# Optimization experiments

Hardware: AMD Instinct MI355X
Metric: run time of the kernel (lower is better)

## Reference

```python
import jax, jax.numpy as jnp
import numpy as np

FEAT = 256
HEADS = 8
HD = FEAT // HEADS
POS = 128
NEG = 128
H = 128
W = 128
B = 8
NSLOT = 512
LN_EPS = 1e-5


def setup_inputs() -> dict:
    key = jax.random.key(0)
    ks = jax.random.split(key, 8)
    HW = H * W
    features = jax.random.normal(ks[0], (HW, B, FEAT), dtype=jnp.float32)
    pos_encodings = jax.random.normal(ks[1], (HW, B, FEAT), dtype=jnp.float32)
    slots = jax.random.normal(ks[2], (1, NSLOT, FEAT), dtype=jnp.float32)
    curio_maps = jax.random.uniform(ks[3], (NSLOT, H, W), dtype=jnp.float32)
    batch_idx = jax.random.randint(ks[4], (NSLOT,), 0, B, dtype=jnp.int32)
    # parameters (xavier-ish scale)
    in_proj_weight = jax.random.normal(ks[5], (3 * FEAT, FEAT), dtype=jnp.float32) * 0.05
    in_proj_bias = jnp.zeros((3 * FEAT,), dtype=jnp.float32)
    out_w = jax.random.normal(ks[6], (FEAT, FEAT), dtype=jnp.float32) * 0.05
    out_b = jnp.zeros((FEAT,), dtype=jnp.float32)
    ln_g = jnp.ones((FEAT,), dtype=jnp.float32)
    ln_b = jnp.zeros((FEAT,), dtype=jnp.float32)
    return {
        'slots': slots, 'features': features, 'pos_encodings': pos_encodings,
        'curio_maps': curio_maps, 'batch_idx': batch_idx,
        'in_proj_weight': in_proj_weight, 'in_proj_bias': in_proj_bias,
        'out_w': out_w, 'out_b': out_b, 'ln_g': ln_g, 'ln_b': ln_b,
        'max_mask_entries': 0,
    }


def _sample_feat_idx(curio_maps, max_mask_entries):
    # curio_maps: [NSLOT, H, W] -> feat_idx: [POS+NEG, NSLOT]
    HW = curio_maps.shape[1] * curio_maps.shape[2]
    flat = curio_maps.reshape(NSLOT, HW)
    sorted_idx = jnp.argsort(-flat, axis=1)  # descending
    pos_idx = sorted_idx[:, :POS]
    pool = sorted_idx[:, POS:HW - max_mask_entries] if max_mask_entries > 0 else sorted_idx[:, POS:]
    # deterministic stand-in for random.sample: evenly-strided negatives
    stride = pool.shape[1] // NEG
    neg_idx = pool[:, ::stride][:, :NEG]
    return jnp.concatenate([pos_idx, neg_idx], axis=1).T  # [S, NSLOT]


def _forward(slots, features, pos_encodings, curio_maps, batch_idx,
             in_proj_weight, in_proj_bias, out_w, out_b, ln_g, ln_b,
             max_mask_entries):
    feat_idx = _sample_feat_idx(curio_maps, max_mask_entries)  # [S, NSLOT]
    S = feat_idx.shape[0]
    qw, kw, vw = in_proj_weight[:FEAT], in_proj_weight[FEAT:2 * FEAT], in_proj_weight[2 * FEAT:]
    qb, kb, vb = in_proj_bias[:FEAT], in_proj_bias[FEAT:2 * FEAT], in_proj_bias[2 * FEAT:]
    scaling = float(HD) ** -0.5
    # sample_type == 'after': project full maps, then gather
    q = (jnp.einsum('bnf,gf->bng', slots, qw) + qb) * scaling       # [1, NSLOT, FEAT]
    k = jnp.einsum('pbf,gf->pbg', features + pos_encodings, kw) + kb  # [HW, B, FEAT]
    v = jnp.einsum('pbf,gf->pbg', features, vw) + vb                  # [HW, B, FEAT]
    kg = k[feat_idx, batch_idx[None, :], :]            # [S, NSLOT, FEAT]
    vg = v[feat_idx[:POS], batch_idx[None, :], :]      # [POS, NSLOT, FEAT]
    qh = q.reshape(NSLOT, HEADS, HD)
    kh = kg.reshape(S, NSLOT, HEADS, HD)
    vh = vg.reshape(POS, NSLOT, HEADS, HD)
    affinities = jnp.einsum('nhd,snhd->snh', qh, kh)   # [S, NSLOT, HEADS]
    attn = jax.nn.softmax(affinities[:POS], axis=0)    # softmax over positive samples
    attn_out = jnp.einsum('pnh,pnhd->nhd', attn, vh).reshape(1, NSLOT, FEAT)
    attn_out = jnp.einsum('bnf,gf->bng', attn_out, out_w) + out_b
    x = slots + attn_out  # dropout is identity in eval
    mu = jnp.mean(x, axis=-1, keepdims=True)
    var = jnp.var(x, axis=-1, keepdims=True)
    new_slots = (x - mu) / jnp.sqrt(var + LN_EPS) * ln_g + ln_b
    return new_slots, affinities


def reference(slots, features, pos_encodings, curio_maps, batch_idx,
              in_proj_weight, in_proj_bias, out_w, out_b, ln_g, ln_b,
              max_mask_entries):
    return _forward(slots, features, pos_encodings, curio_maps, batch_idx,
                    in_proj_weight, in_proj_bias, out_w, out_b, ln_g, ln_b,
                    max_mask_entries)
```

## Files before the change

kernel.cpp:

```cpp
#include <hip/hip_runtime.h>
#include <hip/hip_bf16.h>

#define FEAT 256
#define HEADS 8
#define HD 32
#define POSN 128
#define NEGN 128
#define HWN 16384
#define BN 8
#define NSLOT 512
#define S_TOT 256
#define LN_EPS 1e-5f
#define NBKT 4096
#define AFF_OFF (NSLOT*FEAT)

typedef float f32x4 __attribute__((ext_vector_type(4)));

__global__ __launch_bounds__(256) void k_sample_qkw(const float* __restrict__ curio,
                                                    const int* __restrict__ mme_p,
                                                    const float* __restrict__ slots,
                                                    const float* __restrict__ ipw,
                                                    const float* __restrict__ ipb,
                                                    int* __restrict__ fi_t,
                                                    float* __restrict__ qkw,
                                                    float* __restrict__ qkb)
{
    __shared__ uint32_t hist[NBKT];
    __shared__ uint16_t offs[NBKT];
    __shared__ uint16_t sidx[HWN];
    __shared__ uint32_t ssum[256];
    __shared__ float srow[FEAT];
    __shared__ float qrow[FEAT];
    int slot = blockIdx.x, t = threadIdx.x;
    const float* cm = curio + (size_t)slot * HWN;
    const f32x4* cm4 = (const f32x4*)cm;

    for (int i = t; i < NBKT; i += 256) hist[i] = 0;
    __syncthreads();

    uint32_t bkA[16], bkB[16];
#pragma unroll
    for (int j = 0; j < 16; j++) {
        f32x4 v = cm4[j * 256 + t];
        int b0 = (int)(v[0] * 4096.0f); b0 = b0 < 0 ? 0 : (b0 > NBKT-1 ? NBKT-1 : b0);
        int b1 = (int)(v[1] * 4096.0f); b1 = b1 < 0 ? 0 : (b1 > NBKT-1 ? NBKT-1 : b1);
        int b2 = (int)(v[2] * 4096.0f); b2 = b2 < 0 ? 0 : (b2 > NBKT-1 ? NBKT-1 : b2);
        int b3 = (int)(v[3] * 4096.0f); b3 = b3 < 0 ? 0 : (b3 > NBKT-1 ? NBKT-1 : b3);
        bkA[j] = (uint32_t)b0 | ((uint32_t)b1 << 16);
        bkB[j] = (uint32_t)b2 | ((uint32_t)b3 << 16);
        atomicAdd(&hist[b0], 1u); atomicAdd(&hist[b1], 1u);
        atomicAdd(&hist[b2], 1u); atomicAdd(&hist[b3], 1u);
    }
    __syncthreads();

    uint32_t lsum = 0;
    int base = t * 16;
    for (int j = 0; j < 16; j++) lsum += hist[NBKT-1 - (base + j)];
    ssum[t] = lsum; __syncthreads();
    for (int off = 1; off < 256; off <<= 1) {
        uint32_t v = (t >= off) ? ssum[t - off] : 0u;
        __syncthreads();
        ssum[t] += v;
        __syncthreads();
    }
    uint32_t run = ssum[t] - lsum;
    for (int j = 0; j < 16; j++) {
        int b = NBKT-1 - (base + j);
        offs[b] = (uint16_t)run;
        run += hist[b];
    }
    __syncthreads();
    for (int i = t; i < NBKT; i += 256) hist[i] = 0;
    __syncthreads();

#pragma unroll
    for (int j = 0; j < 16; j++) {
        int idx0 = (j * 256 + t) * 4;
        int b0 = (int)(bkA[j] & 0xFFFFu), b1 = (int)(bkA[j] >> 16);
        int b2 = (int)(bkB[j] & 0xFFFFu), b3 = (int)(bkB[j] >> 16);
        uint32_t p0 = (uint32_t)offs[b0] + atomicAdd(&hist[b0], 1u);
        sidx[p0] = (uint16_t)(idx0 + 0);
        uint32_t p1 = (uint32_t)offs[b1] + atomicAdd(&hist[b1], 1u);
        sidx[p1] = (uint16_t)(idx0 + 1);
        uint32_t p2 = (uint32_t)offs[b2] + atomicAdd(&hist[b2], 1u);
        sidx[p2] = (uint16_t)(idx0 + 2);
        uint32_t p3 = (uint32_t)offs[b3] + atomicAdd(&hist[b3], 1u);
        sidx[p3] = (uint16_t)(idx0 + 3);
    }
    __syncthreads();

    int mme = mme_p[0];
    int stride = (HWN - POSN - mme) / NEGN;
    int r = (t < POSN) ? t : (POSN + stride * (t - POSN));
    int lo = 0, hi = NBKT - 1;
    while (lo < hi) { int mid = (lo + hi) >> 1; if ((int)offs[mid] <= r) hi = mid; else lo = mid + 1; }
    int bkt = lo;
    int start = (int)offs[bkt];
    int cnt   = (int)hist[bkt];
    int rr = r - start;
    int besti = sidx[start + (rr < cnt ? rr : 0)];
    for (int j = 0; j < cnt; j++) {
        int ij = sidx[start + j];
        float vj = cm[ij];
        int rank = 0;
        for (int j2 = 0; j2 < cnt; j2++) {
            int i2 = sidx[start + j2];
            float v2 = cm[i2];
            if (v2 > vj || (v2 == vj && i2 < ij)) rank++;
        }
        if (rank == rr) { besti = ij; break; }
    }
    fi_t[slot * S_TOT + t] = besti;

    __syncthreads();
    srow[t] = slots[slot * FEAT + t];
    __syncthreads();
    {
        const float* qwrow = ipw + (size_t)t * FEAT;
        float acc = 0.f;
#pragma unroll 8
        for (int f = 0; f < FEAT; f++) acc += srow[f] * qwrow[f];
        const float scaling = 0.17677669529663687f;
        qrow[t] = (acc + ipb[t]) * scaling;
    }
    __syncthreads();
    if (t < HEADS) {
        float s = 0.f;
        for (int d = 0; d < HD; d++) s += qrow[t*HD + d] * ipb[FEAT + t*HD + d];
        qkb[slot * HEADS + t] = s;
    }
    const float* kw = ipw + FEAT * FEAT;
    for (int e = t; e < HEADS * FEAT; e += 256) {
        int h = e >> 8, f = e & 255;
        float s = 0.f;
#pragma unroll
        for (int d = 0; d < HD; d++) s += qrow[h*HD + d] * kw[(h*HD + d) * FEAT + f];
        qkw[(size_t)slot * (HEADS*FEAT) + e] = s;
    }
}

__global__ __launch_bounds__(512, 2) void k_attn(const float* __restrict__ features,
                                                 const float* __restrict__ pos_enc,
                                                 const int* __restrict__ batch_idx,
                                                 const int* __restrict__ fi_t,
                                                 const float* __restrict__ qkw,
                                                 const float* __restrict__ qkb,
                                                 const float* __restrict__ slots,
                                                 const float* __restrict__ ipw,
                                                 const float* __restrict__ ipb,
                                                 const float* __restrict__ out_w,
                                                 const float* __restrict__ out_b,
                                                 const float* __restrict__ ln_g,
                                                 const float* __restrict__ ln_b,
                                                 float* __restrict__ aff_out,
                                                 float* __restrict__ out)
{
    __shared__ int   fi_l[S_TOT];
    __shared__ float qkb_l[HEADS];
    __shared__ __align__(16) float affP[POSN][8];
    __shared__ f32x4 wfp[4][HEADS][64];
    __shared__ f32x4 wf4[HEADS][64];
    __shared__ float aoh[512];
    __shared__ __align__(16) float ao_l[FEAT];
    __shared__ float xgh[512];
    __shared__ float r1[4], r2[4];

    int n = blockIdx.x, t = threadIdx.x, lane = t & 63, w = t >> 6;
    if (t < S_TOT) fi_l[t] = fi_t[n * S_TOT + t];
    if (t < HEADS) qkb_l[t] = qkb[n * HEADS + t];
    int b = batch_idx[n];

    const float* qk = qkw + (size_t)n * (HEADS*FEAT) + 4 * lane;
    f32x4 qw0 = *(const f32x4*)(qk + 0*FEAT);
    f32x4 qw1 = *(const f32x4*)(qk + 1*FEAT);
    f32x4 qw2 = *(const f32x4*)(qk + 2*FEAT);
    f32x4 qw3 = *(const f32x4*)(qk + 3*FEAT);
    f32x4 qw4 = *(const f32x4*)(qk + 4*FEAT);
    f32x4 qw5 = *(const f32x4*)(qk + 5*FEAT);
    f32x4 qw6 = *(const f32x4*)(qk + 6*FEAT);
    f32x4 qw7 = *(const f32x4*)(qk + 7*FEAT);
    __syncthreads();
    float qb = qkb_l[lane & 7];
    int b0 = lane & 1, b1 = (lane >> 1) & 1, b2 = (lane >> 2) & 1;

    auto dorow = [&](int p, f32x4 cf, f32x4 cg) {
        float x0 = cf[0]+cg[0], x1 = cf[1]+cg[1], x2 = cf[2]+cg[2], x3 = cf[3]+cg[3];
        float p0 = x0*qw0[0] + x1*qw0[1] + x2*qw0[2] + x3*qw0[3];
        float p1 = x0*qw1[0] + x1*qw1[1] + x2*qw1[2] + x3*qw1[3];
        float p2 = x0*qw2[0] + x1*qw2[1] + x2*qw2[2] + x3*qw2[3];
        float p3 = x0*qw3[0] + x1*qw3[1] + x2*qw3[2] + x3*qw3[3];
        float p4 = x0*qw4[0] + x1*qw4[1] + x2*qw4[2] + x3*qw4[3];
        float p5 = x0*qw5[0] + x1*qw5[1] + x2*qw5[2] + x3*qw5[3];
        float p6 = x0*qw6[0] + x1*qw6[1] + x2*qw6[2] + x3*qw6[3];
        float p7 = x0*qw7[0] + x1*qw7[1] + x2*qw7[2] + x3*qw7[3];
        float s0 = b0 ? p0 : p1, s1 = b0 ? p2 : p3, s2 = b0 ? p4 : p5, s3 = b0 ? p6 : p7;
        float a0 = (b0 ? p1 : p0) + __shfl_xor(s0, 1);
        float a1 = (b0 ? p3 : p2) + __shfl_xor(s1, 1);
        float a2 = (b0 ? p5 : p4) + __shfl_xor(s2, 1);
        float a3 = (b0 ? p7 : p6) + __shfl_xor(s3, 1);
        float u0 = b1 ? a0 : a1, u1 = b1 ? a2 : a3;
        float c0 = (b1 ? a1 : a0) + __shfl_xor(u0, 2);
        float c1 = (b1 ? a3 : a2) + __shfl_xor(u1, 2);
        float u2 = b2 ? c0 : c1;
        float d = (b2 ? c1 : c0) + __shfl_xor(u2, 4);
        d += __shfl_xor(d, 8);
        d += __shfl_xor(d, 16);
        d += __shfl_xor(d, 32);
        d += qb;
        if (lane < 8) {
            aff_out[(size_t)p * (NSLOT*HEADS) + n*HEADS + lane] = d;
            if (p < POSN) affP[p][lane] = d;
        }
    };

    f32x4 cache[16];
    size_t base0 = ((size_t)fi_l[w] * BN + b) * FEAT + 4 * lane;
    f32x4 f4 = *(const f32x4*)(features + base0);
    f32x4 g4 = *(const f32x4*)(pos_enc + base0);
#pragma unroll
    for (int i = 0; i < 16; i++) {
        f32x4 cf = f4, cg = g4;
        {
            size_t nb = ((size_t)fi_l[w + 8*(i+1)] * BN + b) * FEAT + 4 * lane;
            f4 = *(const f32x4*)(features + nb);
            g4 = *(const f32x4*)(pos_enc + nb);
        }
        cache[i] = cf;
        dorow(w + 8*i, cf, cg);
    }
#pragma unroll 4
    for (int i = 16; i < 32; i++) {
        f32x4 cf = f4, cg = g4;
        if (i < 31) {
            size_t nb = ((size_t)fi_l[w + 8*(i+1)] * BN + b) * FEAT + 4 * lane;
            f4 = *(const f32x4*)(features + nb);
            g4 = *(const f32x4*)(pos_enc + nb);
        }
        dorow(w + 8*i, cf, cg);
    }
    __syncthreads();

    if (t < 256) {
        int h = t >> 5, l = t & 31;
        float v0 = affP[l][h], v1 = affP[l+32][h], v2 = affP[l+64][h], v3 = affP[l+96][h];
        float m = fmaxf(fmaxf(v0, v1), fmaxf(v2, v3));
        for (int off = 16; off > 0; off >>= 1) m = fmaxf(m, __shfl_xor(m, off, 32));
        float e0 = expf(v0 - m), e1 = expf(v1 - m), e2 = expf(v2 - m), e3 = expf(v3 - m);
        float s = e0 + e1 + e2 + e3;
        for (int off = 16; off > 0; off >>= 1) s += __shfl_xor(s, off, 32);
        float inv = 1.0f / s;
        affP[l][h] = e0*inv; affP[l+32][h] = e1*inv; affP[l+64][h] = e2*inv; affP[l+96][h] = e3*inv;
    }
    __syncthreads();

    {
        f32x4 acc[8];
#pragma unroll
        for (int h = 0; h < 8; h++) acc[h] = (f32x4){0.f,0.f,0.f,0.f};
#pragma unroll
        for (int i = 0; i < 16; i++) {
            int p = w + 8*i;
            const f32x4* ap = (const f32x4*)&affP[p][0];
            f32x4 a03 = ap[0], a47 = ap[1];
            acc[0] += cache[i] * a03[0];
            acc[1] += cache[i] * a03[1];
            acc[2] += cache[i] * a03[2];
            acc[3] += cache[i] * a03[3];
            acc[4] += cache[i] * a47[0];
            acc[5] += cache[i] * a47[1];
            acc[6] += cache[i] * a47[2];
            acc[7] += cache[i] * a47[3];
        }
        if (w < 4) {
#pragma unroll
            for (int h = 0; h < 8; h++) wfp[w][h][lane] = acc[h];
        }
        __syncthreads();
        if (w >= 4) {
#pragma unroll
            for (int h = 0; h < 8; h++) wfp[w-4][h][lane] += acc[h];
        }
        __syncthreads();
    }
    {
        int h = t >> 6, q2 = t & 63;
        f32x4 s = wfp[0][h][q2] + wfp[1][h][q2] + wfp[2][h][q2] + wfp[3][h][q2];
        wf4[h][q2] = s;
    }
    __syncthreads();

    {
        int g = t & 255, half = t >> 8;
        const float* vwrow = ipw + (size_t)(2*FEAT + g) * FEAT + half*128;
        const f32x4* wfv = &wf4[g >> 5][half*32];
        float s = 0.f;
#pragma unroll 8
        for (int f4i = 0; f4i < 32; f4i++) {
            f32x4 wv = *(const f32x4*)(vwrow + 4*f4i);
            f32x4 y = wfv[f4i];
            s += wv[0]*y[0] + wv[1]*y[1] + wv[2]*y[2] + wv[3]*y[3];
        }
        aoh[t] = s;
    }
    __syncthreads();
    if (t < 256) ao_l[t] = aoh[t] + aoh[t + 256] + ipb[2*FEAT + t];
    __syncthreads();

    {
        int g = t & 255, half = t >> 8;
        const float* owrow = out_w + (size_t)g * FEAT + half*128;
        const f32x4* av = (const f32x4*)&ao_l[half*128];
        float s = 0.f;
#pragma unroll 8
        for (int f4i = 0; f4i < 32; f4i++) {
            f32x4 wv = *(const f32x4*)(owrow + 4*f4i);
            f32x4 y = av[f4i];
            s += wv[0]*y[0] + wv[1]*y[1] + wv[2]*y[2] + wv[3]*y[3];
        }
        xgh[t] = s;
    }
    __syncthreads();

    float xg = 0.f;
    if (t < 256) {
        xg = xgh[t] + xgh[t + 256] + out_b[t] + slots[n * FEAT + t];
        float s1 = xg, s2 = xg * xg;
        for (int off = 32; off > 0; off >>= 1) {
            s1 += __shfl_xor(s1, off);
            s2 += __shfl_xor(s2, off);
        }
        if ((t & 63) == 0) { r1[t >> 6] = s1; r2[t >> 6] = s2; }
    }
    __syncthreads();
    if (t < 256) {
        float sum1 = r1[0] + r1[1] + r1[2] + r1[3];
        float sum2 = r2[0] + r2[1] + r2[2] + r2[3];
        float mu  = sum1 * (1.0f / FEAT);
        float var = sum2 * (1.0f / FEAT) - mu * mu;
        float nrm = (xg - mu) * rsqrtf(var + LN_EPS);
        out[n * FEAT + t] = nrm * ln_g[t] + ln_b[t];
    }
}

extern "C" void kernel_launch(void* const* d_in, const int* in_sizes, int n_in,
                              void* d_out, int out_size, void* d_ws, size_t ws_size,
                              hipStream_t stream)
{
    (void)in_sizes; (void)n_in; (void)out_size; (void)ws_size;
    const float* slots    = (const float*)d_in[0];
    const float* features = (const float*)d_in[1];
    const float* pos_enc  = (const float*)d_in[2];
    const float* curio    = (const float*)d_in[3];
    const int*   batch_idx= (const int*)d_in[4];
    const float* ipw      = (const float*)d_in[5];
    const float* ipb      = (const float*)d_in[6];
    const float* out_w    = (const float*)d_in[7];
    const float* out_b    = (const float*)d_in[8];
    const float* ln_g     = (const float*)d_in[9];
    const float* ln_b     = (const float*)d_in[10];
    const int*   mme      = (const int*)d_in[11];
    float* out = (float*)d_out;

    char* ws = (char*)d_ws;
    int*   fi_t = (int*)ws;
    float* qkw  = (float*)(ws + (512 << 10));
    float* qkb  = (float*)(ws + (512 << 10) + (4 << 20));
    float* aff  = out + AFF_OFF;

    hipLaunchKernelGGL(k_sample_qkw, dim3(NSLOT), dim3(256), 0, stream,
                       curio, mme, slots, ipw, ipb, fi_t, qkw, qkb);
    hipLaunchKernelGGL(k_attn, dim3(NSLOT), dim3(512), 0, stream,
                       features, pos_enc, batch_idx, fi_t, qkw, qkb, slots, ipw, ipb,
                       out_w, out_b, ln_g, ln_b, aff, out);
}
```

Measured before the change: 132.6 us.

## Split attention kernel into positive and negative sample blocks per slot

The attention kernel now launches two blocks per slot. One block computes the affinities for the 128 negative samples and exits early, while the other handles the positive samples, softmax, value aggregation and layer norm. The gather loop is also restructured to keep two rows of loads in flight instead of one. This doubles parallelism and shortens the per-block critical path. The cost is redundant setup loads per block and extra pressure on registers and shared memory.

```diff
diff --git a/kernel.cpp b/kernel.cpp
--- a/kernel.cpp
+++ b/kernel.cpp
@@ -165,7 +165,9 @@
     __shared__ float xgh[512];
     __shared__ float r1[4], r2[4];
 
-    int n = blockIdx.x, t = threadIdx.x, lane = t & 63, w = t >> 6;
+    int bid = blockIdx.x;
+    int n = bid >> 1, kind = bid & 1;
+    int t = threadIdx.x, lane = t & 63, w = t >> 6;
     if (t < S_TOT) fi_l[t] = fi_t[n * S_TOT + t];
     if (t < HEADS) qkb_l[t] = qkb[n * HEADS + t];
     int b = batch_idx[n];
@@ -213,30 +215,57 @@
         }
     };
 
+    auto rowaddr = [&](int s) {
+        return ((size_t)fi_l[s] * BN + b) * FEAT + 4 * lane;
+    };
+
+    if (kind) {
+        int base_s = POSN + w;
+        size_t aA = rowaddr(base_s);
+        size_t aB = rowaddr(base_s + 8);
+        f32x4 fA = *(const f32x4*)(features + aA), gA = *(const f32x4*)(pos_enc + aA);
+        f32x4 fB = *(const f32x4*)(features + aB), gB = *(const f32x4*)(pos_enc + aB);
+#pragma unroll
+        for (int i = 0; i < 16; i += 2) {
+            f32x4 cf = fA, cg = gA;
+            if (i + 2 < 16) {
+                size_t nb = rowaddr(base_s + 8*(i+2));
+                fA = *(const f32x4*)(features + nb); gA = *(const f32x4*)(pos_enc + nb);
+            }
+            dorow(base_s + 8*i, cf, cg);
+            f32x4 cf2 = fB, cg2 = gB;
+            if (i + 3 < 16) {
+                size_t nb = rowaddr(base_s + 8*(i+3));
+                fB = *(const f32x4*)(features + nb); gB = *(const f32x4*)(pos_enc + nb);
+            }
+            dorow(base_s + 8*(i+1), cf2, cg2);
+        }
+        return;
+    }
+
     f32x4 cache[16];
-    size_t base0 = ((size_t)fi_l[w] * BN + b) * FEAT + 4 * lane;
-    f32x4 f4 = *(const f32x4*)(features + base0);
-    f32x4 g4 = *(const f32x4*)(pos_enc + base0);
-#pragma unroll
-    for (int i = 0; i < 16; i++) {
-        f32x4 cf = f4, cg = g4;
-        {
-            size_t nb = ((size_t)fi_l[w + 8*(i+1)] * BN + b) * FEAT + 4 * lane;
-            f4 = *(const f32x4*)(features + nb);
-            g4 = *(const f32x4*)(pos_enc + nb);
-        }
-        cache[i] = cf;
-        dorow(w + 8*i, cf, cg);
-    }
-#pragma unroll 4
-    for (int i = 16; i < 32; i++) {
-        f32x4 cf = f4, cg = g4;
-        if (i < 31) {
-            size_t nb = ((size_t)fi_l[w + 8*(i+1)] * BN + b) * FEAT + 4 * lane;
-            f4 = *(const f32x4*)(features + nb);
-            g4 = *(const f32x4*)(pos_enc + nb);
-        }
-        dorow(w + 8*i, cf, cg);
+    {
+        size_t aA = rowaddr(w);
+        size_t aB = rowaddr(w + 8);
+        f32x4 fA = *(const f32x4*)(features + aA), gA = *(const f32x4*)(pos_enc + aA);
+        f32x4 fB = *(const f32x4*)(features + aB), gB = *(const f32x4*)(pos_enc + aB);
+#pragma unroll
+        for (int i = 0; i < 16; i += 2) {
+            f32x4 cf = fA, cg = gA;
+            if (i + 2 < 16) {
+                size_t nb = rowaddr(w + 8*(i+2));
+                fA = *(const f32x4*)(features + nb); gA = *(const f32x4*)(pos_enc + nb);
+            }
+            cache[i] = cf;
+            dorow(w + 8*i, cf, cg);
+            f32x4 cf2 = fB, cg2 = gB;
+            if (i + 3 < 16) {
+                size_t nb = rowaddr(w + 8*(i+3));
+                fB = *(const f32x4*)(features + nb); gB = *(const f32x4*)(pos_enc + nb);
+            }
+            cache[i+1] = cf2;
+            dorow(w + 8*(i+1), cf2, cg2);
+        }
     }
     __syncthreads();
 
@@ -369,7 +398,7 @@
 
     hipLaunchKernelGGL(k_sample_qkw, dim3(NSLOT), dim3(256), 0, stream,
                        curio, mme, slots, ipw, ipb, fi_t, qkw, qkb);
-    hipLaunchKernelGGL(k_attn, dim3(NSLOT), dim3(512), 0, stream,
+    hipLaunchKernelGGL(k_attn, dim3(2 * NSLOT), dim3(512), 0, stream,
                        features, pos_enc, batch_idx, fi_t, qkw, qkb, slots, ipw, ipb,
                        out_w, out_b, ln_g, ln_b, aff, out);
 }
```

New measurement: 166.1 us. 25.2% more time.

## Invert affinity gather into streaming pass over feature rows with bucketed requests

Applied to the files above, without the earlier changes.

Rather than each slot block gathering 256 random feature and pos_enc rows, the sampling kernel now records, for every (pixel, batch) key, the list of (slot, sample) requests. A new streaming kernel walks all feature rows in order, loads each requested row once and computes the affinity for every request attached to it. Requests beyond the per-key capacity go through a spill list. The output kernel then reloads the affinities and the positive feature rows. The aim is to turn scattered, duplicated gathers into coalesced sequential reads with reuse. The cost is global atomics, two memsets, an extra kernel launch and extra aff round-trips, and the stream pass scans all 131k keys even though many have no requests.

```diff
diff --git a/kernel.cpp b/kernel.cpp
--- a/kernel.cpp
+++ b/kernel.cpp
@@ -13,6 +13,12 @@
 #define LN_EPS 1e-5f
 #define NBKT 4096
 #define AFF_OFF (NSLOT*FEAT)
+#define NKEY (HWN*BN)
+#define CAP 16
+#define SPILL_MAX 4096
+#define ROWS_PER_WAVE 8
+#define STREAM_ROW_BLOCKS 4096
+#define SPILL_BLOCKS 8
 
 typedef float f32x4 __attribute__((ext_vector_type(4)));
 
@@ -21,14 +27,19 @@
                                                     const float* __restrict__ slots,
                                                     const float* __restrict__ ipw,
                                                     const float* __restrict__ ipb,
+                                                    const int* __restrict__ batch_idx,
                                                     int* __restrict__ fi_t,
                                                     float* __restrict__ qkw,
-                                                    float* __restrict__ qkb)
+                                                    float* __restrict__ qkb,
+                                                    unsigned int* __restrict__ counts,
+                                                    unsigned int* __restrict__ entries,
+                                                    unsigned int* __restrict__ spill_cnt,
+                                                    unsigned long long* __restrict__ spills)
 {
-    __shared__ uint32_t hist[NBKT];
+    __shared__ unsigned int hist[NBKT];
     __shared__ uint16_t offs[NBKT];
     __shared__ uint16_t sidx[HWN];
-    __shared__ uint32_t ssum[256];
+    __shared__ unsigned int ssum[256];
     __shared__ float srow[FEAT];
     __shared__ float qrow[FEAT];
     int slot = blockIdx.x, t = threadIdx.x;
@@ -38,7 +49,7 @@
     for (int i = t; i < NBKT; i += 256) hist[i] = 0;
     __syncthreads();
 
-    uint32_t bkA[16], bkB[16];
+    unsigned int bkA[16], bkB[16];
 #pragma unroll
     for (int j = 0; j < 16; j++) {
         f32x4 v = cm4[j * 256 + t];
@@ -46,24 +57,24 @@
         int b1 = (int)(v[1] * 4096.0f); b1 = b1 < 0 ? 0 : (b1 > NBKT-1 ? NBKT-1 : b1);
         int b2 = (int)(v[2] * 4096.0f); b2 = b2 < 0 ? 0 : (b2 > NBKT-1 ? NBKT-1 : b2);
         int b3 = (int)(v[3] * 4096.0f); b3 = b3 < 0 ? 0 : (b3 > NBKT-1 ? NBKT-1 : b3);
-        bkA[j] = (uint32_t)b0 | ((uint32_t)b1 << 16);
-        bkB[j] = (uint32_t)b2 | ((uint32_t)b3 << 16);
+        bkA[j] = (unsigned int)b0 | ((unsigned int)b1 << 16);
+        bkB[j] = (unsigned int)b2 | ((unsigned int)b3 << 16);
         atomicAdd(&hist[b0], 1u); atomicAdd(&hist[b1], 1u);
         atomicAdd(&hist[b2], 1u); atomicAdd(&hist[b3], 1u);
     }
     __syncthreads();
 
-    uint32_t lsum = 0;
+    unsigned int lsum = 0;
     int base = t * 16;
     for (int j = 0; j < 16; j++) lsum += hist[NBKT-1 - (base + j)];
     ssum[t] = lsum; __syncthreads();
     for (int off = 1; off < 256; off <<= 1) {
-        uint32_t v = (t >= off) ? ssum[t - off] : 0u;
+        unsigned int v = (t >= off) ? ssum[t - off] : 0u;
         __syncthreads();
         ssum[t] += v;
         __syncthreads();
     }
-    uint32_t run = ssum[t] - lsum;
+    unsigned int run = ssum[t] - lsum;
     for (int j = 0; j < 16; j++) {
         int b = NBKT-1 - (base + j);
         offs[b] = (uint16_t)run;
@@ -78,13 +89,13 @@
         int idx0 = (j * 256 + t) * 4;
         int b0 = (int)(bkA[j] & 0xFFFFu), b1 = (int)(bkA[j] >> 16);
         int b2 = (int)(bkB[j] & 0xFFFFu), b3 = (int)(bkB[j] >> 16);
-        uint32_t p0 = (uint32_t)offs[b0] + atomicAdd(&hist[b0], 1u);
+        unsigned int p0 = (unsigned int)offs[b0] + atomicAdd(&hist[b0], 1u);
         sidx[p0] = (uint16_t)(idx0 + 0);
-        uint32_t p1 = (uint32_t)offs[b1] + atomicAdd(&hist[b1], 1u);
+        unsigned int p1 = (unsigned int)offs[b1] + atomicAdd(&hist[b1], 1u);
         sidx[p1] = (uint16_t)(idx0 + 1);
-        uint32_t p2 = (uint32_t)offs[b2] + atomicAdd(&hist[b2], 1u);
+        unsigned int p2 = (unsigned int)offs[b2] + atomicAdd(&hist[b2], 1u);
         sidx[p2] = (uint16_t)(idx0 + 2);
-        uint32_t p3 = (uint32_t)offs[b3] + atomicAdd(&hist[b3], 1u);
+        unsigned int p3 = (unsigned int)offs[b3] + atomicAdd(&hist[b3], 1u);
         sidx[p3] = (uint16_t)(idx0 + 3);
     }
     __syncthreads();
@@ -112,6 +123,20 @@
     }
     fi_t[slot * S_TOT + t] = besti;
 
+    {
+        int b = batch_idx[slot];
+        int key = besti * BN + b;
+        unsigned int payload = ((unsigned int)slot << 8) | (unsigned int)t;
+        unsigned int c = atomicAdd(&counts[key], 1u);
+        if (c < CAP) {
+            entries[(size_t)key * CAP + c] = payload;
+        } else {
+            unsigned int sp = atomicAdd(spill_cnt, 1u);
+            if (sp < SPILL_MAX)
+                spills[sp] = ((unsigned long long)payload << 32) | (unsigned int)key;
+        }
+    }
+
     __syncthreads();
     srow[t] = slots[slot * FEAT + t];
     __syncthreads();
@@ -139,37 +164,13 @@
     }
 }
 
-__global__ __launch_bounds__(512, 2) void k_attn(const float* __restrict__ features,
-                                                 const float* __restrict__ pos_enc,
-                                                 const int* __restrict__ batch_idx,
-                                                 const int* __restrict__ fi_t,
-                                                 const float* __restrict__ qkw,
-                                                 const float* __restrict__ qkb,
-                                                 const float* __restrict__ slots,
-                                                 const float* __restrict__ ipw,
-                                                 const float* __restrict__ ipb,
-                                                 const float* __restrict__ out_w,
-                                                 const float* __restrict__ out_b,
-                                                 const float* __restrict__ ln_g,
-                                                 const float* __restrict__ ln_b,
-                                                 float* __restrict__ aff_out,
-                                                 float* __restrict__ out)
+__device__ __forceinline__ void ref_affinity(const float* __restrict__ qkw,
+                                             const float* __restrict__ qkb,
+                                             float* __restrict__ aff_out,
+                                             f32x4 xs, unsigned int payload,
+                                             int lane, int b0, int b1, int b2)
 {
-    __shared__ int   fi_l[S_TOT];
-    __shared__ float qkb_l[HEADS];
-    __shared__ __align__(16) float affP[POSN][8];
-    __shared__ f32x4 wfp[4][HEADS][64];
-    __shared__ f32x4 wf4[HEADS][64];
-    __shared__ float aoh[512];
-    __shared__ __align__(16) float ao_l[FEAT];
-    __shared__ float xgh[512];
-    __shared__ float r1[4], r2[4];
-
-    int n = blockIdx.x, t = threadIdx.x, lane = t & 63, w = t >> 6;
-    if (t < S_TOT) fi_l[t] = fi_t[n * S_TOT + t];
-    if (t < HEADS) qkb_l[t] = qkb[n * HEADS + t];
-    int b = batch_idx[n];
-
+    int n = (int)(payload >> 8), s = (int)(payload & 255u);
     const float* qk = qkw + (size_t)n * (HEADS*FEAT) + 4 * lane;
     f32x4 qw0 = *(const f32x4*)(qk + 0*FEAT);
     f32x4 qw1 = *(const f32x4*)(qk + 1*FEAT);
@@ -179,66 +180,152 @@
     f32x4 qw5 = *(const f32x4*)(qk + 5*FEAT);
     f32x4 qw6 = *(const f32x4*)(qk + 6*FEAT);
     f32x4 qw7 = *(const f32x4*)(qk + 7*FEAT);
-    __syncthreads();
-    float qb = qkb_l[lane & 7];
+    float qb = qkb[n * HEADS + (lane & 7)];
+    float p0 = xs[0]*qw0[0] + xs[1]*qw0[1] + xs[2]*qw0[2] + xs[3]*qw0[3];
+    float p1 = xs[0]*qw1[0] + xs[1]*qw1[1] + xs[2]*qw1[2] + xs[3]*qw1[3];
+    float p2 = xs[0]*qw2[0] + xs[1]*qw2[1] + xs[2]*qw2[2] + xs[3]*qw2[3];
+    float p3 = xs[0]*qw3[0] + xs[1]*qw3[1] + xs[2]*qw3[2] + xs[3]*qw3[3];
+    float p4 = xs[0]*qw4[0] + xs[1]*qw4[1] + xs[2]*qw4[2] + xs[3]*qw4[3];
+    float p5 = xs[0]*qw5[0] + xs[1]*qw5[1] + xs[2]*qw5[2] + xs[3]*qw5[3];
+    float p6 = xs[0]*qw6[0] + xs[1]*qw6[1] + xs[2]*qw6[2] + xs[3]*qw6[3];
+    float p7 = xs[0]*qw7[0] + xs[1]*qw7[1] + xs[2]*qw7[2] + xs[3]*qw7[3];
+    float s0 = b0 ? p0 : p1, s1 = b0 ? p2 : p3, s2 = b0 ? p4 : p5, s3 = b0 ? p6 : p7;
+    float a0 = (b0 ? p1 : p0) + __shfl_xor(s0, 1);
+    float a1 = (b0 ? p3 : p2) + __shfl_xor(s1, 1);
+    float a2 = (b0 ? p5 : p4) + __shfl_xor(s2, 1);
+    float a3 = (b0 ? p7 : p6) + __shfl_xor(s3, 1);
+    float u0 = b1 ? a0 : a1, u1 = b1 ? a2 : a3;
+    float c0 = (b1 ? a1 : a0) + __shfl_xor(u0, 2);
+    float c1 = (b1 ? a3 : a2) + __shfl_xor(u1, 2);
+    float u2 = b2 ? c0 : c1;
+    float d = (b2 ? c1 : c0) + __shfl_xor(u2, 4);
+    d += __shfl_xor(d, 8);
+    d += __shfl_xor(d, 16);
+    d += __shfl_xor(d, 32);
+    d += qb;
+    if (lane < 8)
+        aff_out[(size_t)s * (NSLOT*HEADS) + n*HEADS + lane] = d;
+}
+
+__global__ __launch_bounds__(256) void k_stream_aff(const float* __restrict__ features,
+                                                    const float* __restrict__ pos_enc,
+                                                    const float* __restrict__ qkw,
+                                                    const float* __restrict__ qkb,
+                                                    const unsigned int* __restrict__ counts,
+                                                    const unsigned int* __restrict__ entries,
+                                                    const unsigned int* __restrict__ spill_cnt,
+                                                    const unsigned long long* __restrict__ spills,
+                                                    float* __restrict__ aff_out)
+{
+    int t = threadIdx.x, lane = t & 63, w = t >> 6;
     int b0 = lane & 1, b1 = (lane >> 1) & 1, b2 = (lane >> 2) & 1;
 
-    auto dorow = [&](int p, f32x4 cf, f32x4 cg) {
-        float x0 = cf[0]+cg[0], x1 = cf[1]+cg[1], x2 = cf[2]+cg[2], x3 = cf[3]+cg[3];
-        float p0 = x0*qw0[0] + x1*qw0[1] + x2*qw0[2] + x3*qw0[3];
-        float p1 = x0*qw1[0] + x1*qw1[1] + x2*qw1[2] + x3*qw1[3];
-        float p2 = x0*qw2[0] + x1*qw2[1] + x2*qw2[2] + x3*qw2[3];
-        float p3 = x0*qw3[0] + x1*qw3[1] + x2*qw3[2] + x3*qw3[3];
-        float p4 = x0*qw4[0] + x1*qw4[1] + x2*qw4[2] + x3*qw4[3];
-        float p5 = x0*qw5[0] + x1*qw5[1] + x2*qw5[2] + x3*qw5[3];
-        float p6 = x0*qw6[0] + x1*qw6[1] + x2*qw6[2] + x3*qw6[3];
-        float p7 = x0*qw7[0] + x1*qw7[1] + x2*qw7[2] + x3*qw7[3];
-        float s0 = b0 ? p0 : p1, s1 = b0 ? p2 : p3, s2 = b0 ? p4 : p5, s3 = b0 ? p6 : p7;
-        float a0 = (b0 ? p1 : p0) + __shfl_xor(s0, 1);
-        float a1 = (b0 ? p3 : p2) + __shfl_xor(s1, 1);
-        float a2 = (b0 ? p5 : p4) + __shfl_xor(s2, 1);
-        float a3 = (b0 ? p7 : p6) + __shfl_xor(s3, 1);
-        float u0 = b1 ? a0 : a1, u1 = b1 ? a2 : a3;
-        float c0 = (b1 ? a1 : a0) + __shfl_xor(u0, 2);
-        float c1 = (b1 ? a3 : a2) + __shfl_xor(u1, 2);
-        float u2 = b2 ? c0 : c1;
-        float d = (b2 ? c1 : c0) + __shfl_xor(u2, 4);
-        d += __shfl_xor(d, 8);
-        d += __shfl_xor(d, 16);
-        d += __shfl_xor(d, 32);
-        d += qb;
-        if (lane < 8) {
-            aff_out[(size_t)p * (NSLOT*HEADS) + n*HEADS + lane] = d;
-            if (p < POSN) affP[p][lane] = d;
-        }
-    };
+    if (blockIdx.x >= STREAM_ROW_BLOCKS) {
+        unsigned int nsp = *spill_cnt;
+        if (nsp > SPILL_MAX) nsp = SPILL_MAX;
+        unsigned int start = (blockIdx.x - STREAM_ROW_BLOCKS) * 4 + w;
+        for (unsigned int k = start; k < nsp; k += SPILL_BLOCKS * 4) {
+            unsigned long long e = spills[k];
+            unsigned int key = (unsigned int)e;
+            unsigned int payload = (unsigned int)(e >> 32);
+            const float* fp = features + (size_t)key * FEAT + 4 * lane;
+            const float* gp = pos_enc  + (size_t)key * FEAT + 4 * lane;
+            f32x4 cf = *(const f32x4*)fp;
+            f32x4 cg = *(const f32x4*)gp;
+            ref_affinity(qkw, qkb, aff_out, cf + cg, payload, lane, b0, b1, b2);
+        }
+        return;
+    }
+
+    int gw = blockIdx.x * 4 + w;
+    int r0 = gw * ROWS_PER_WAVE;
+
+    int takes[ROWS_PER_WAVE];
+#pragma unroll
+    for (int i = 0; i < ROWS_PER_WAVE; i++) {
+        unsigned int c = counts[r0 + i];
+        takes[i] = (int)(c < CAP ? c : CAP);
+    }
+
+    int cur = 0;
+    while (cur < ROWS_PER_WAVE && takes[cur] == 0) cur++;
+    f32x4 f4 = {0,0,0,0}, g4 = {0,0,0,0};
+    if (cur < ROWS_PER_WAVE) {
+        const float* fp = features + (size_t)(r0 + cur) * FEAT + 4 * lane;
+        const float* gp = pos_enc  + (size_t)(r0 + cur) * FEAT + 4 * lane;
+        f4 = *(const f32x4*)fp; g4 = *(const f32x4*)gp;
+    }
+    while (cur < ROWS_PER_WAVE) {
+        int nx = cur + 1;
+        while (nx < ROWS_PER_WAVE && takes[nx] == 0) nx++;
+        f32x4 cf = f4, cg = g4;
+        if (nx < ROWS_PER_WAVE) {
+            const float* fp = features + (size_t)(r0 + nx) * FEAT + 4 * lane;
+            const float* gp = pos_enc  + (size_t)(r0 + nx) * FEAT + 4 * lane;
+            f4 = *(const f32x4*)fp; g4 = *(const f32x4*)gp;
+        }
+        f32x4 xs = cf + cg;
+        const unsigned int* ebase = entries + (size_t)(r0 + cur) * CAP;
+        int tk = takes[cur];
+        for (int j = 0; j < tk; j++)
+            ref_affinity(qkw, qkb, aff_out, xs, ebase[j], lane, b0, b1, b2);
+        cur = nx;
+    }
+}
+
+__global__ __launch_bounds__(512, 2) void k_out(const float* __restrict__ features,
+                                                const int* __restrict__ batch_idx,
+                                                const int* __restrict__ fi_t,
+                                                const float* __restrict__ slots,
+                                                const float* __restrict__ ipw,
+                                                const float* __restrict__ ipb,
+                                                const float* __restrict__ out_w,
+                                                const float* __restrict__ out_b,
+                                                const float* __restrict__ ln_g,
+                                                const float* __restrict__ ln_b,
+                                                const float* __restrict__ aff,
+                                                float* __restrict__ out)
+{
+    __shared__ int   fiP[POSN];
+    __shared__ __align__(16) float affP[POSN][8];
+    __shared__ f32x4 wfp[4][HEADS][64];
+    __shared__ f32x4 wf4[HEADS][64];
+    __shared__ float aoh[512];
+    __shared__ __align__(16) float ao_l[FEAT];
+    __shared__ float xgh[512];
+    __shared__ float r1[4], r2[4];
+
+    int n = blockIdx.x, t = threadIdx.x, lane = t & 63, w = t >> 6;
+    if (t < POSN) fiP[t] = fi_t[n * S_TOT + t];
+    for (int e = t; e < POSN * HEADS; e += 512) {
+        int p = e >> 3, h = e & 7;
+        affP[p][h] = aff[(size_t)p * (NSLOT*HEADS) + n*HEADS + h];
+    }
+    int b = batch_idx[n];
+    __syncthreads();
 
     f32x4 cache[16];
-    size_t base0 = ((size_t)fi_l[w] * BN + b) * FEAT + 4 * lane;
-    f32x4 f4 = *(const f32x4*)(features + base0);
-    f32x4 g4 = *(const f32x4*)(pos_enc + base0);
-#pragma unroll
-    for (int i = 0; i < 16; i++) {
-        f32x4 cf = f4, cg = g4;
-        {
-            size_t nb = ((size_t)fi_l[w + 8*(i+1)] * BN + b) * FEAT + 4 * lane;
-            f4 = *(const f32x4*)(features + nb);
-            g4 = *(const f32x4*)(pos_enc + nb);
-        }
-        cache[i] = cf;
-        dorow(w + 8*i, cf, cg);
-    }
-#pragma unroll 4
-    for (int i = 16; i < 32; i++) {
-        f32x4 cf = f4, cg = g4;
-        if (i < 31) {
-            size_t nb = ((size_t)fi_l[w + 8*(i+1)] * BN + b) * FEAT + 4 * lane;
-            f4 = *(const f32x4*)(features + nb);
-            g4 = *(const f32x4*)(pos_enc + nb);
-        }
-        dorow(w + 8*i, cf, cg);
-    }
-    __syncthreads();
+    {
+        size_t aA = ((size_t)fiP[w] * BN + b) * FEAT + 4 * lane;
+        size_t aB = ((size_t)fiP[w + 8] * BN + b) * FEAT + 4 * lane;
+        f32x4 fA = *(const f32x4*)(features + aA);
+        f32x4 fB = *(const f32x4*)(features + aB);
+#pragma unroll
+        for (int i = 0; i < 16; i += 2) {
+            f32x4 c0 = fA;
+            if (i + 2 < 16) {
+                size_t nb = ((size_t)fiP[w + 8*(i+2)] * BN + b) * FEAT + 4 * lane;
+                fA = *(const f32x4*)(features + nb);
+            }
+            cache[i] = c0;
+            f32x4 c1 = fB;
+            if (i + 3 < 16) {
+                size_t nb = ((size_t)fiP[w + 8*(i+3)] * BN + b) * FEAT + 4 * lane;
+                fB = *(const f32x4*)(features + nb);
+            }
+            cache[i+1] = c1;
+        }
+    }
 
     if (t < 256) {
         int h = t >> 5, l = t & 31;
@@ -362,14 +449,31 @@
     float* out = (float*)d_out;
 
     char* ws = (char*)d_ws;
+    const size_t OFF_QKW = 512u << 10;
+    const size_t OFF_QKB = OFF_QKW + (4u << 20);
+    const size_t OFF_CNT = OFF_QKB + (64u << 10);
+    const size_t OFF_ENT = OFF_CNT + (512u << 10);
+    const size_t OFF_SPC = OFF_ENT + ((size_t)NKEY * CAP * 4);
+    const size_t OFF_SPL = OFF_SPC + 1024;
+
     int*   fi_t = (int*)ws;
-    float* qkw  = (float*)(ws + (512 << 10));
-    float* qkb  = (float*)(ws + (512 << 10) + (4 << 20));
+    float* qkw  = (float*)(ws + OFF_QKW);
+    float* qkb  = (float*)(ws + OFF_QKB);
+    unsigned int* counts = (unsigned int*)(ws + OFF_CNT);
+    unsigned int* entries = (unsigned int*)(ws + OFF_ENT);
+    unsigned int* spill_cnt = (unsigned int*)(ws + OFF_SPC);
+    unsigned long long* spills = (unsigned long long*)(ws + OFF_SPL);
     float* aff  = out + AFF_OFF;
 
+    hipMemsetAsync(counts, 0, (512u << 10) + 0, stream);
+    hipMemsetAsync(spill_cnt, 0, 1024, stream);
+
     hipLaunchKernelGGL(k_sample_qkw, dim3(NSLOT), dim3(256), 0, stream,
-                       curio, mme, slots, ipw, ipb, fi_t, qkw, qkb);
-    hipLaunchKernelGGL(k_attn, dim3(NSLOT), dim3(512), 0, stream,
-                       features, pos_enc, batch_idx, fi_t, qkw, qkb, slots, ipw, ipb,
+                       curio, mme, slots, ipw, ipb, batch_idx,
+                       fi_t, qkw, qkb, counts, entries, spill_cnt, spills);
+    hipLaunchKernelGGL(k_stream_aff, dim3(STREAM_ROW_BLOCKS + SPILL_BLOCKS), dim3(256), 0, stream,
+                       features, pos_enc, qkw, qkb, counts, entries, spill_cnt, spills, aff);
+    hipLaunchKernelGGL(k_out, dim3(NSLOT), dim3(512), 0, stream,
+                       features, batch_idx, fi_t, slots, ipw, ipb,
                        out_w, out_b, ln_g, ln_b, aff, out);
 }
```

After: 177.9 us. 34.2% more time.

## Split attention kernel into affinity and output kernels with deeper prefetch

Applied to the files above, without the earlier changes.

Splits the fused attention kernel into two. The first computes all 256 affinities per slot over a 2x512 grid of 256-thread blocks, using a double-buffered four-row prefetch. The second reads the positive affinities back from global memory, re-gathers the feature rows it needs for the value path, and then does softmax, output projection and layernorm. The aim is more parallelism and more memory-level parallelism in the gather-heavy affinity stage. In exchange it adds a kernel launch, a global round-trip of the affinities, and a second gather of the positive feature rows.

```diff
diff --git a/kernel.cpp b/kernel.cpp
--- a/kernel.cpp
+++ b/kernel.cpp
@@ -25,10 +25,10 @@
                                                     float* __restrict__ qkw,
                                                     float* __restrict__ qkb)
 {
-    __shared__ uint32_t hist[NBKT];
+    __shared__ unsigned int hist[NBKT];
     __shared__ uint16_t offs[NBKT];
     __shared__ uint16_t sidx[HWN];
-    __shared__ uint32_t ssum[256];
+    __shared__ unsigned int ssum[256];
     __shared__ float srow[FEAT];
     __shared__ float qrow[FEAT];
     int slot = blockIdx.x, t = threadIdx.x;
@@ -38,7 +38,7 @@
     for (int i = t; i < NBKT; i += 256) hist[i] = 0;
     __syncthreads();
 
-    uint32_t bkA[16], bkB[16];
+    unsigned int bkA[16], bkB[16];
 #pragma unroll
     for (int j = 0; j < 16; j++) {
         f32x4 v = cm4[j * 256 + t];
@@ -46,24 +46,24 @@
         int b1 = (int)(v[1] * 4096.0f); b1 = b1 < 0 ? 0 : (b1 > NBKT-1 ? NBKT-1 : b1);
         int b2 = (int)(v[2] * 4096.0f); b2 = b2 < 0 ? 0 : (b2 > NBKT-1 ? NBKT-1 : b2);
         int b3 = (int)(v[3] * 4096.0f); b3 = b3 < 0 ? 0 : (b3 > NBKT-1 ? NBKT-1 : b3);
-        bkA[j] = (uint32_t)b0 | ((uint32_t)b1 << 16);
-        bkB[j] = (uint32_t)b2 | ((uint32_t)b3 << 16);
+        bkA[j] = (unsigned int)b0 | ((unsigned int)b1 << 16);
+        bkB[j] = (unsigned int)b2 | ((unsigned int)b3 << 16);
         atomicAdd(&hist[b0], 1u); atomicAdd(&hist[b1], 1u);
         atomicAdd(&hist[b2], 1u); atomicAdd(&hist[b3], 1u);
     }
     __syncthreads();
 
-    uint32_t lsum = 0;
+    unsigned int lsum = 0;
     int base = t * 16;
     for (int j = 0; j < 16; j++) lsum += hist[NBKT-1 - (base + j)];
     ssum[t] = lsum; __syncthreads();
     for (int off = 1; off < 256; off <<= 1) {
-        uint32_t v = (t >= off) ? ssum[t - off] : 0u;
+        unsigned int v = (t >= off) ? ssum[t - off] : 0u;
         __syncthreads();
         ssum[t] += v;
         __syncthreads();
     }
-    uint32_t run = ssum[t] - lsum;
+    unsigned int run = ssum[t] - lsum;
     for (int j = 0; j < 16; j++) {
         int b = NBKT-1 - (base + j);
         offs[b] = (uint16_t)run;
@@ -78,13 +78,13 @@
         int idx0 = (j * 256 + t) * 4;
         int b0 = (int)(bkA[j] & 0xFFFFu), b1 = (int)(bkA[j] >> 16);
         int b2 = (int)(bkB[j] & 0xFFFFu), b3 = (int)(bkB[j] >> 16);
-        uint32_t p0 = (uint32_t)offs[b0] + atomicAdd(&hist[b0], 1u);
+        unsigned int p0 = (unsigned int)offs[b0] + atomicAdd(&hist[b0], 1u);
         sidx[p0] = (uint16_t)(idx0 + 0);
-        uint32_t p1 = (uint32_t)offs[b1] + atomicAdd(&hist[b1], 1u);
+        unsigned int p1 = (unsigned int)offs[b1] + atomicAdd(&hist[b1], 1u);
         sidx[p1] = (uint16_t)(idx0 + 1);
-        uint32_t p2 = (uint32_t)offs[b2] + atomicAdd(&hist[b2], 1u);
+        unsigned int p2 = (unsigned int)offs[b2] + atomicAdd(&hist[b2], 1u);
         sidx[p2] = (uint16_t)(idx0 + 2);
-        uint32_t p3 = (uint32_t)offs[b3] + atomicAdd(&hist[b3], 1u);
+        unsigned int p3 = (unsigned int)offs[b3] + atomicAdd(&hist[b3], 1u);
         sidx[p3] = (uint16_t)(idx0 + 3);
     }
     __syncthreads();
@@ -139,34 +139,20 @@
     }
 }
 
-__global__ __launch_bounds__(512, 2) void k_attn(const float* __restrict__ features,
-                                                 const float* __restrict__ pos_enc,
-                                                 const int* __restrict__ batch_idx,
-                                                 const int* __restrict__ fi_t,
-                                                 const float* __restrict__ qkw,
-                                                 const float* __restrict__ qkb,
-                                                 const float* __restrict__ slots,
-                                                 const float* __restrict__ ipw,
-                                                 const float* __restrict__ ipb,
-                                                 const float* __restrict__ out_w,
-                                                 const float* __restrict__ out_b,
-                                                 const float* __restrict__ ln_g,
-                                                 const float* __restrict__ ln_b,
-                                                 float* __restrict__ aff_out,
-                                                 float* __restrict__ out)
+__global__ __launch_bounds__(256) void k_aff(const float* __restrict__ features,
+                                             const float* __restrict__ pos_enc,
+                                             const int* __restrict__ batch_idx,
+                                             const int* __restrict__ fi_t,
+                                             const float* __restrict__ qkw,
+                                             const float* __restrict__ qkb,
+                                             float* __restrict__ aff_out)
 {
-    __shared__ int   fi_l[S_TOT];
+    __shared__ int   fi_l[128];
     __shared__ float qkb_l[HEADS];
-    __shared__ __align__(16) float affP[POSN][8];
-    __shared__ f32x4 wfp[4][HEADS][64];
-    __shared__ f32x4 wf4[HEADS][64];
-    __shared__ float aoh[512];
-    __shared__ __align__(16) float ao_l[FEAT];
-    __shared__ float xgh[512];
-    __shared__ float r1[4], r2[4];
-
-    int n = blockIdx.x, t = threadIdx.x, lane = t & 63, w = t >> 6;
-    if (t < S_TOT) fi_l[t] = fi_t[n * S_TOT + t];
+    int n = blockIdx.y, q = blockIdx.x;
+    int t = threadIdx.x, lane = t & 63, w = t >> 6;
+
+    if (t < 128) fi_l[t] = fi_t[n * S_TOT + q * 128 + t];
     if (t < HEADS) qkb_l[t] = qkb[n * HEADS + t];
     int b = batch_idx[n];
 
@@ -183,16 +169,15 @@
     float qb = qkb_l[lane & 7];
     int b0 = lane & 1, b1 = (lane >> 1) & 1, b2 = (lane >> 2) & 1;
 
-    auto dorow = [&](int p, f32x4 cf, f32x4 cg) {
-        float x0 = cf[0]+cg[0], x1 = cf[1]+cg[1], x2 = cf[2]+cg[2], x3 = cf[3]+cg[3];
-        float p0 = x0*qw0[0] + x1*qw0[1] + x2*qw0[2] + x3*qw0[3];
-        float p1 = x0*qw1[0] + x1*qw1[1] + x2*qw1[2] + x3*qw1[3];
-        float p2 = x0*qw2[0] + x1*qw2[1] + x2*qw2[2] + x3*qw2[3];
-        float p3 = x0*qw3[0] + x1*qw3[1] + x2*qw3[2] + x3*qw3[3];
-        float p4 = x0*qw4[0] + x1*qw4[1] + x2*qw4[2] + x3*qw4[3];
-        float p5 = x0*qw5[0] + x1*qw5[1] + x2*qw5[2] + x3*qw5[3];
-        float p6 = x0*qw6[0] + x1*qw6[1] + x2*qw6[2] + x3*qw6[3];
-        float p7 = x0*qw7[0] + x1*qw7[1] + x2*qw7[2] + x3*qw7[3];
+    auto dorow = [&](int s, f32x4 x) {
+        float p0 = x[0]*qw0[0] + x[1]*qw0[1] + x[2]*qw0[2] + x[3]*qw0[3];
+        float p1 = x[0]*qw1[0] + x[1]*qw1[1] + x[2]*qw1[2] + x[3]*qw1[3];
+        float p2 = x[0]*qw2[0] + x[1]*qw2[1] + x[2]*qw2[2] + x[3]*qw2[3];
+        float p3 = x[0]*qw3[0] + x[1]*qw3[1] + x[2]*qw3[2] + x[3]*qw3[3];
+        float p4 = x[0]*qw4[0] + x[1]*qw4[1] + x[2]*qw4[2] + x[3]*qw4[3];
+        float p5 = x[0]*qw5[0] + x[1]*qw5[1] + x[2]*qw5[2] + x[3]*qw5[3];
+        float p6 = x[0]*qw6[0] + x[1]*qw6[1] + x[2]*qw6[2] + x[3]*qw6[3];
+        float p7 = x[0]*qw7[0] + x[1]*qw7[1] + x[2]*qw7[2] + x[3]*qw7[3];
         float s0 = b0 ? p0 : p1, s1 = b0 ? p2 : p3, s2 = b0 ? p4 : p5, s3 = b0 ? p6 : p7;
         float a0 = (b0 ? p1 : p0) + __shfl_xor(s0, 1);
         float a1 = (b0 ? p3 : p2) + __shfl_xor(s1, 1);
@@ -207,38 +192,75 @@
         d += __shfl_xor(d, 16);
         d += __shfl_xor(d, 32);
         d += qb;
-        if (lane < 8) {
-            aff_out[(size_t)p * (NSLOT*HEADS) + n*HEADS + lane] = d;
-            if (p < POSN) affP[p][lane] = d;
-        }
+        if (lane < 8)
+            aff_out[(size_t)s * (NSLOT*HEADS) + n*HEADS + lane] = d;
     };
 
+    int sbase = w * 32;
+
+    f32x4 fbuf[2][4], gbuf[2][4];
+#pragma unroll
+    for (int j = 0; j < 4; j++) {
+        size_t a_ = ((size_t)fi_l[sbase + j] * BN + b) * FEAT + 4 * lane;
+        fbuf[0][j] = *(const f32x4*)(features + a_);
+        gbuf[0][j] = *(const f32x4*)(pos_enc + a_);
+    }
+#pragma unroll
+    for (int bi = 0; bi < 8; bi++) {
+        const int cur = bi & 1, nxt = cur ^ 1;
+        if (bi < 7) {
+#pragma unroll
+            for (int j = 0; j < 4; j++) {
+                size_t a_ = ((size_t)fi_l[sbase + (bi+1)*4 + j] * BN + b) * FEAT + 4 * lane;
+                fbuf[nxt][j] = *(const f32x4*)(features + a_);
+                gbuf[nxt][j] = *(const f32x4*)(pos_enc + a_);
+            }
+        }
+#pragma unroll
+        for (int r = 0; r < 4; r++) {
+            f32x4 x = fbuf[cur][r] + gbuf[cur][r];
+            dorow(q * 128 + sbase + bi*4 + r, x);
+        }
+    }
+}
+
+__global__ __launch_bounds__(512) void k_out(const float* __restrict__ features,
+                                             const int* __restrict__ batch_idx,
+                                             const int* __restrict__ fi_t,
+                                             const float* __restrict__ slots,
+                                             const float* __restrict__ ipw,
+                                             const float* __restrict__ ipb,
+                                             const float* __restrict__ out_w,
+                                             const float* __restrict__ out_b,
+                                             const float* __restrict__ ln_g,
+                                             const float* __restrict__ ln_b,
+                                             const float* __restrict__ aff,
+                                             float* __restrict__ out)
+{
+    __shared__ int   fiP[POSN];
+    __shared__ __align__(16) float affP[POSN][8];
+    __shared__ f32x4 wfp[4][HEADS][64];
+    __shared__ f32x4 wf4[HEADS][64];
+    __shared__ float aoh[512];
+    __shared__ __align__(16) float ao_l[FEAT];
+    __shared__ float xgh[512];
+    __shared__ float r1[4], r2[4];
+
+    int n = blockIdx.x, t = threadIdx.x, lane = t & 63, w = t >> 6;
+    if (t < POSN) fiP[t] = fi_t[n * S_TOT + t];
+    for (int e = t; e < POSN * HEADS; e += 512) {
+        int p = e >> 3, h = e & 7;
+        affP[p][h] = aff[(size_t)p * (NSLOT*HEADS) + n*HEADS + h];
+    }
+    int b = batch_idx[n];
+    __syncthreads();
+
     f32x4 cache[16];
-    size_t base0 = ((size_t)fi_l[w] * BN + b) * FEAT + 4 * lane;
-    f32x4 f4 = *(const f32x4*)(features + base0);
-    f32x4 g4 = *(const f32x4*)(pos_enc + base0);
 #pragma unroll
     for (int i = 0; i < 16; i++) {
-        f32x4 cf = f4, cg = g4;
-        {
-            size_t nb = ((size_t)fi_l[w + 8*(i+1)] * BN + b) * FEAT + 4 * lane;
-            f4 = *(const f32x4*)(features + nb);
-            g4 = *(const f32x4*)(pos_enc + nb);
-        }
-        cache[i] = cf;
-        dorow(w + 8*i, cf, cg);
-    }
-#pragma unroll 4
-    for (int i = 16; i < 32; i++) {
-        f32x4 cf = f4, cg = g4;
-        if (i < 31) {
-            size_t nb = ((size_t)fi_l[w + 8*(i+1)] * BN + b) * FEAT + 4 * lane;
-            f4 = *(const f32x4*)(features + nb);
-            g4 = *(const f32x4*)(pos_enc + nb);
-        }
-        dorow(w + 8*i, cf, cg);
-    }
-    __syncthreads();
+        size_t a_ = ((size_t)fiP[w + 8*i] * BN + b) * FEAT + 4 * lane;
+        cache[i] = *(const f32x4*)(features + a_);
+    }
 
     if (t < 256) {
         int h = t >> 5, l = t & 31;
@@ -369,7 +391,9 @@
 
     hipLaunchKernelGGL(k_sample_qkw, dim3(NSLOT), dim3(256), 0, stream,
                        curio, mme, slots, ipw, ipb, fi_t, qkw, qkb);
-    hipLaunchKernelGGL(k_attn, dim3(NSLOT), dim3(512), 0, stream,
-                       features, pos_enc, batch_idx, fi_t, qkw, qkb, slots, ipw, ipb,
+    hipLaunchKernelGGL(k_aff, dim3(2, NSLOT), dim3(256), 0, stream,
+                       features, pos_enc, batch_idx, fi_t, qkw, qkb, aff);
+    hipLaunchKernelGGL(k_out, dim3(NSLOT), dim3(512), 0, stream,
+                       features, batch_idx, fi_t, slots, ipw, ipb,
                        out_w, out_b, ln_g, ln_b, aff, out);
 }
```

Result: slower. 139.6 us (+5.3%).
